# Performance work log

Hardware: AMD Instinct MI355X
Metric: run time of the kernel (lower is better)

## Reference

```python
import jax, jax.numpy as jnp
import numpy as np
from jax import lax

# db5 (Daubechies-10) reconstruction lowpass filter, same values as pywt.Wavelet('db5').rec_lo
REC_LO = jnp.array([
    0.160102397974125,
    0.6038292697974729,
    0.7243085284385744,
    0.13842814590110342,
    -0.24229488706619015,
    -0.03224486958502952,
    0.07757149384006515,
    -0.006241490213011705,
    -0.012580751999015526,
    0.003335725285001549,
], dtype=jnp.float32)
DEC_LO = REC_LO[::-1]  # decomposition lowpass = reversed rec_lo
F = 10  # db5 filter length


def setup_inputs() -> dict:
    key = jax.random.key(0)
    x = jax.random.normal(key, (64, 128, 4096), dtype=jnp.float32)
    return {"x": x}


def reference(x) -> jnp.ndarray:
    # x: (B, C, L) -> flatten(1,2) -> (B, N) with N = C*L
    B, C, L = x.shape
    sig = x.reshape(B, 1, C * L)  # NCH layout, single channel

    # ---- DWT (db5, symmetric mode), lowpass branch only (cD is discarded upstream) ----
    # pywt equivalence: cA = np.convolve(pad(x, F-1, 'symmetric'), dec_lo, 'valid')[1::2]
    # np.convolve with dec_lo == correlation with rec_lo; offset-1 stride-2 downsampling
    ext = jnp.pad(sig, ((0, 0), (0, 0), (F - 1, F - 1)), mode="symmetric")
    k_dec = REC_LO.reshape(1, 1, F)
    cA = lax.conv_general_dilated(
        ext[:, :, 1:], k_dec,
        window_strides=(2,), padding=[(0, 0)],
        dimension_numbers=("NCH", "OIH", "NCH"),
    )  # (B, 1, (N+F-1)//2)

    # ---- IDWT from cA only: ya = pywt.idwt(cA, None, 'db5', 'smooth') ----
    # upsample by 2 (length 2*Nc-1), full-convolve with rec_lo, trim F-2 from each side
    # => transposed conv: lhs_dilation=2, correlation kernel = reversed rec_lo, pad (1,1)
    k_rec = DEC_LO.reshape(1, 1, F)
    ya = lax.conv_general_dilated(
        cA, k_rec,
        window_strides=(1,), padding=[(1, 1)], lhs_dilation=(2,),
        dimension_numbers=("NCH", "OIH", "NCH"),
    )  # (B, 1, 2*Nc - F + 2) -- matches torch .unsqueeze(1) output layout
    return ya
```

## Files before the change

### kernel.cpp

```cpp
#include <hip/hip_runtime.h>


typedef float f2 __attribute__((ext_vector_type(2)));

#define L_SIG 524288
#define SPAN  2048
#define HALF  1024

constexpr float RL[10] = {
    0.160102397974125f,   0.6038292697974729f,  0.7243085284385744f,
    0.13842814590110342f, -0.24229488706619015f, -0.03224486958502952f,
    0.07757149384006515f, -0.006241490213011705f, -0.012580751999015526f,
    0.003335725285001549f};

struct Coef { float we[18]; float wo[18]; };

constexpr Coef make_coef() {
    Coef c{};
    for (int d = 0; d < 18; ++d) {
        float se = 0.f, so = 0.f;
        for (int j = 0; j < 5; ++j) {
            int i = d - 2 * j;
            if (i >= 0 && i < 10) {
                se += RL[8 - 2 * j] * RL[i];
                so += RL[9 - 2 * j] * RL[i];
            }
        }
        c.we[d] = se;
        c.wo[d] = so;
    }
    return c;
}

constexpr Coef CF = make_coef();

__global__ __launch_bounds__(256)
void wavelet_pk_kernel(const float* __restrict__ x, float* __restrict__ out) {
    const int batch = blockIdx.y;
    const int p0    = blockIdx.x * SPAN;
    const float* xb = x   + (size_t)batch * L_SIG;
    float*       ob = out + (size_t)batch * L_SIG;

    const int t  = threadIdx.x;
    const int qA = p0 + 4 * t;
    const int qB = qA + HALF;

    float wA[20], wB[20];

    const bool edge = (blockIdx.x == 0) || (blockIdx.x == gridDim.x - 1);
    if (edge) {
#pragma unroll
        for (int i = 0; i < 20; ++i) {
            int ka = qA + i - 8;
            int kb = qB + i - 8;
            ka = (ka < 0) ? (-1 - ka) : ((ka >= L_SIG) ? (2 * L_SIG - 1 - ka) : ka);
            kb = (kb < 0) ? (-1 - kb) : ((kb >= L_SIG) ? (2 * L_SIG - 1 - kb) : kb);
            wA[i] = xb[ka];
            wB[i] = xb[kb];
        }
    } else {
        const float4* a4 = (const float4*)(xb + qA - 8);
        const float4* b4 = (const float4*)(xb + qB - 8);
#pragma unroll
        for (int r = 0; r < 5; ++r) {
            float4 fa = a4[r];
            float4 fb = b4[r];
            wA[4 * r + 0] = fa.x; wA[4 * r + 1] = fa.y;
            wA[4 * r + 2] = fa.z; wA[4 * r + 3] = fa.w;
            wB[4 * r + 0] = fb.x; wB[4 * r + 1] = fb.y;
            wB[4 * r + 2] = fb.z; wB[4 * r + 3] = fb.w;
        }
    }

    f2 u[20];
#pragma unroll
    for (int i = 0; i < 20; ++i) {
        f2 p; p[0] = wA[i]; p[1] = wB[i];
        u[i] = p;
    }

    f2 e0 = 0.f, d1 = 0.f, e2 = 0.f, d3 = 0.f;
#pragma unroll
    for (int d = 0; d < 18; ++d) {
        e0 += CF.we[d] * u[d];
        d1 += CF.wo[d] * u[d];
        e2 += CF.we[d] * u[d + 2];
        d3 += CF.wo[d] * u[d + 2];
    }

    float4 oa = make_float4(e0[0], d1[0], e2[0], d3[0]);
    float4 obv = make_float4(e0[1], d1[1], e2[1], d3[1]);
    *((float4*)(ob + qA)) = oa;
    *((float4*)(ob + qB)) = obv;
}

extern "C" void kernel_launch(void* const* d_in, const int* in_sizes, int n_in,
                              void* d_out, int out_size, void* d_ws, size_t ws_size,
                              hipStream_t stream) {
    const float* x = (const float*)d_in[0];
    float* out     = (float*)d_out;

    const int B = in_sizes[0] / L_SIG;
    dim3 grid(L_SIG / SPAN, B);
    wavelet_pk_kernel<<<grid, 256, 0, stream>>>(x, out);
}
```

Measured before the change: 234.0 us.

## Compute 16 contiguous outputs per thread with shared halo and nontemporal stores

Each thread now produces 16 contiguous outputs from a 36-element register window instead of two separate 4-output groups, each needing its own 20-element window. This cuts redundant halo loads from 2.5x to about 2.25x. The accumulation is restructured so each coefficient pair (even/odd) is applied as a packed f2 multiply-add across 8 accumulators. Outputs are written with nontemporal stores to reduce cache pollution. The trade-offs are higher register pressure, strided per-thread float4 loads (16-float stride across lanes) that coalesce less well, and fewer blocks in the grid.

```diff
diff --git a/kernel.cpp b/kernel.cpp
--- a/kernel.cpp
+++ b/kernel.cpp
@@ -2,10 +2,11 @@
 
 
 typedef float f2 __attribute__((ext_vector_type(2)));
+typedef float f4 __attribute__((ext_vector_type(4)));
 
 #define L_SIG 524288
-#define SPAN  2048
-#define HALF  1024
+#define T_OUT 16
+#define SPAN  (256 * T_OUT)
 
 constexpr float RL[10] = {
     0.160102397974125f,   0.6038292697974729f,  0.7243085284385744f,
@@ -35,63 +36,55 @@
 constexpr Coef CF = make_coef();
 
 __global__ __launch_bounds__(256)
-void wavelet_pk_kernel(const float* __restrict__ x, float* __restrict__ out) {
+void wavelet_v3_kernel(const float* __restrict__ x, float* __restrict__ out) {
     const int batch = blockIdx.y;
     const int p0    = blockIdx.x * SPAN;
     const float* xb = x   + (size_t)batch * L_SIG;
     float*       ob = out + (size_t)batch * L_SIG;
 
-    const int t  = threadIdx.x;
-    const int qA = p0 + 4 * t;
-    const int qB = qA + HALF;
+    const int q = p0 + T_OUT * threadIdx.x;
 
-    float wA[20], wB[20];
+    float w[36];
 
     const bool edge = (blockIdx.x == 0) || (blockIdx.x == gridDim.x - 1);
     if (edge) {
 #pragma unroll
-        for (int i = 0; i < 20; ++i) {
-            int ka = qA + i - 8;
-            int kb = qB + i - 8;
-            ka = (ka < 0) ? (-1 - ka) : ((ka >= L_SIG) ? (2 * L_SIG - 1 - ka) : ka);
-            kb = (kb < 0) ? (-1 - kb) : ((kb >= L_SIG) ? (2 * L_SIG - 1 - kb) : kb);
-            wA[i] = xb[ka];
-            wB[i] = xb[kb];
+        for (int i = 0; i < 36; ++i) {
+            int k = q - 8 + i;
+            k = (k < 0) ? (-1 - k) : ((k >= L_SIG) ? (2 * L_SIG - 1 - k) : k);
+            w[i] = xb[k];
         }
     } else {
-        const float4* a4 = (const float4*)(xb + qA - 8);
-        const float4* b4 = (const float4*)(xb + qB - 8);
+        const f4* a4 = (const f4*)(xb + q - 8);
 #pragma unroll
-        for (int r = 0; r < 5; ++r) {
-            float4 fa = a4[r];
-            float4 fb = b4[r];
-            wA[4 * r + 0] = fa.x; wA[4 * r + 1] = fa.y;
-            wA[4 * r + 2] = fa.z; wA[4 * r + 3] = fa.w;
-            wB[4 * r + 0] = fb.x; wB[4 * r + 1] = fb.y;
-            wB[4 * r + 2] = fb.z; wB[4 * r + 3] = fb.w;
+        for (int r = 0; r < 9; ++r) {
+            f4 f = a4[r];
+            w[4 * r + 0] = f.x; w[4 * r + 1] = f.y;
+            w[4 * r + 2] = f.z; w[4 * r + 3] = f.w;
         }
     }
 
-    f2 u[20];
+    f2 acc[8];
 #pragma unroll
-    for (int i = 0; i < 20; ++i) {
-        f2 p; p[0] = wA[i]; p[1] = wB[i];
-        u[i] = p;
+    for (int k = 0; k < 8; ++k) acc[k] = (f2)0.f;
+
+#pragma unroll
+    for (int d = 0; d < 18; ++d) {
+        f2 cf; cf[0] = CF.we[d]; cf[1] = CF.wo[d];
+#pragma unroll
+        for (int k = 0; k < 8; ++k) {
+            acc[k] += cf * w[2 * k + d];
+        }
     }
 
-    f2 e0 = 0.f, d1 = 0.f, e2 = 0.f, d3 = 0.f;
+    f4* o4 = (f4*)(ob + q);
 #pragma unroll
-    for (int d = 0; d < 18; ++d) {
-        e0 += CF.we[d] * u[d];
-        d1 += CF.wo[d] * u[d];
-        e2 += CF.we[d] * u[d + 2];
-        d3 += CF.wo[d] * u[d + 2];
+    for (int k = 0; k < 4; ++k) {
+        f4 o;
+        o.x = acc[2 * k][0];     o.y = acc[2 * k][1];
+        o.z = acc[2 * k + 1][0]; o.w = acc[2 * k + 1][1];
+        __builtin_nontemporal_store(o, o4 + k);
     }
-
-    float4 oa = make_float4(e0[0], d1[0], e2[0], d3[0]);
-    float4 obv = make_float4(e0[1], d1[1], e2[1], d3[1]);
-    *((float4*)(ob + qA)) = oa;
-    *((float4*)(ob + qB)) = obv;
 }
 
 extern "C" void kernel_launch(void* const* d_in, const int* in_sizes, int n_in,
@@ -102,5 +95,5 @@
 
     const int B = in_sizes[0] / L_SIG;
     dim3 grid(L_SIG / SPAN, B);
-    wavelet_pk_kernel<<<grid, 256, 0, stream>>>(x, out);
+    wavelet_v3_kernel<<<grid, 256, 0, stream>>>(x, out);
 }
```

Measured after the change: 279.6 us. +19.5%, slower.
